# Optimization experiments

Measured on AMD Instinct MI355X. Metric: run time of the kernel, lower is better.

Reference implementation:

```python
import jax, jax.numpy as jnp
from jax import lax
import numpy as np
import math

N = 8
IN_CH = 3
EPS = 1e-6


def _dct_basis(n=N):
    # basis[u, i] = c(u) * cos(pi * u * (i + 0.5) / n)
    u = np.arange(n)
    i = np.arange(n)
    b = np.cos(np.pi * np.outer(u, i + 0.5) / n)
    c = np.full(n, math.sqrt(2.0 / n))
    c[0] = math.sqrt(1.0 / n)
    return b * c[:, None]


def _dct_conv_weight(n=N, in_ch=IN_CH):
    # weight[k = u*n + v, i, j] = basis[u,i] * basis[v,j]; grouped conv OIHW with I=1
    b = _dct_basis(n)
    w = np.einsum('ui,vj->uvij', b, b).reshape(n * n, 1, n, n).astype(np.float32)
    return np.concatenate([w] * in_ch, axis=0)  # [in_ch*n*n, 1, n, n]


def setup_inputs() -> dict:
    key = jax.random.key(0)
    k1, k2, k3 = jax.random.split(key, 3)
    B, C, H, W = 32, 3, 512, 512
    x = jax.random.uniform(k1, (B, C, H, W), dtype=jnp.float32)  # RGB in [0,1)
    # per-(sample, channel) stats; keep divisor d = max - min + eps > 1 so the
    # B-times repeated in-place normalization of the original stays finite
    max_ = 1.5 + jax.random.uniform(k2, (B, C * N * N, 1, 1), dtype=jnp.float32)
    min_ = 0.1 * jax.random.uniform(k3, (B, C * N * N, 1, 1), dtype=jnp.float32)
    ycbcr_w = jnp.asarray(
        [[0.299, 0.587, 0.114],
         [-0.169, -0.331, 0.5],
         [0.5, -0.419, -0.081]], dtype=jnp.float32)  # [out_c, in_c]
    dct_w = jnp.asarray(_dct_conv_weight())  # [192, 1, 8, 8]
    return {"x": x, "max_": max_, "min_": min_, "ycbcr_w": ycbcr_w, "dct_w": dct_w}


def reference(x, max_, min_, ycbcr_w, dct_w):
    # 1x1 RGB -> YCbCr conv == channel matmul
    ycbcr = jnp.einsum('oc,bchw->bohw', ycbcr_w, x)
    # grouped 8x8 stride-8 block-DCT conv: [B, 192, H/8, W/8]
    dct = lax.conv_general_dilated(
        ycbcr, dct_w, window_strides=(N, N), padding='VALID',
        feature_group_count=IN_CH,
        dimension_numbers=('NCHW', 'OIHW', 'NCHW'))
    # Original applies t = (t - min) / (max - min + eps) in-place B times per
    # sample (outer loop index i is unused but repeats the whole inner loop).
    d = max_ - min_ + EPS
    B = x.shape[0]
    out = lax.fori_loop(0, B, lambda i, t: (t - min_) / d, dct)
    return out
```

## Files before the change

### kernel.cpp

```cpp
#include <hip/hip_runtime.h>


#define HW 512
#define CHST (HW * HW)
#define NPAIR 6144
#define EPS 1e-6f

static constexpr float BASIS[8][8] = {
  { 0.35355339059327373f, 0.35355339059327373f, 0.35355339059327373f, 0.35355339059327373f,
    0.35355339059327373f, 0.35355339059327373f, 0.35355339059327373f, 0.35355339059327373f },
  { 0.49039264020161522f, 0.41573480615127262f, 0.27778511650980114f, 0.09754516100806412f,
   -0.09754516100806412f,-0.27778511650980114f,-0.41573480615127262f,-0.49039264020161522f },
  { 0.46193976625564337f, 0.19134171618254492f,-0.19134171618254492f,-0.46193976625564337f,
   -0.46193976625564337f,-0.19134171618254492f, 0.19134171618254492f, 0.46193976625564337f },
  { 0.41573480615127262f,-0.09754516100806412f,-0.49039264020161522f,-0.27778511650980114f,
    0.27778511650980114f, 0.49039264020161522f, 0.09754516100806412f,-0.41573480615127262f },
  { 0.35355339059327373f,-0.35355339059327373f,-0.35355339059327373f, 0.35355339059327373f,
    0.35355339059327373f,-0.35355339059327373f,-0.35355339059327373f, 0.35355339059327373f },
  { 0.27778511650980114f,-0.49039264020161522f, 0.09754516100806412f, 0.41573480615127262f,
   -0.41573480615127262f,-0.09754516100806412f, 0.49039264020161522f,-0.27778511650980114f },
  { 0.19134171618254492f,-0.46193976625564337f, 0.46193976625564337f,-0.19134171618254492f,
   -0.19134171618254492f, 0.46193976625564337f,-0.46193976625564337f, 0.19134171618254492f },
  { 0.09754516100806412f,-0.27778511650980114f, 0.41573480615127262f,-0.49039264020161522f,
    0.49039264020161522f,-0.41573480615127262f, 0.27778511650980114f,-0.09754516100806412f }
};

__global__ void precomp_norm(const float* __restrict__ max_,
                             const float* __restrict__ min_,
                             float* __restrict__ so) {
    int i = blockIdx.x * 256 + threadIdx.x;
    if (i >= NPAIR) return;
    float mn = min_[i], mx = max_[i];
    float d = mx - mn + EPS;
    float a = 1.0f / d;
    float a2 = a * a, a4 = a2 * a2, a8 = a4 * a4, a16 = a8 * a8, a32 = a16 * a16;
    float geo = a * (1.0f - a32) / (1.0f - a);
    so[2 * i]     = a32;
    so[2 * i + 1] = -mn * geo;
}

template <bool USE_WS>
__global__ __launch_bounds__(256)
void dct_kernel(const float* __restrict__ x,
                const float* __restrict__ ycbcr_w,
                const float* __restrict__ so,
                const float* __restrict__ max_,
                const float* __restrict__ min_,
                float* __restrict__ out) {
    __shared__ float ylds[3 * 8 * HW];

    const int b  = blockIdx.x >> 6;
    const int by = blockIdx.x & 63;
    const int t  = threadIdx.x;

    const float* band = x + (size_t)(b * 3) * CHST + (by * 8) * HW;

    float w00 = ycbcr_w[0], w01 = ycbcr_w[1], w02 = ycbcr_w[2];
    float w10 = ycbcr_w[3], w11 = ycbcr_w[4], w12 = ycbcr_w[5];
    float w20 = ycbcr_w[6], w21 = ycbcr_w[7], w22 = ycbcr_w[8];

    float4 Rv[4], Gv[4], Bv[4];
#pragma unroll
    for (int w = 0; w < 4; ++w) {
        const int o = t + 256 * w;
        Rv[w] = ((const float4*)(band))[o];
        Gv[w] = ((const float4*)(band + CHST))[o];
        Bv[w] = ((const float4*)(band + 2 * CHST))[o];
    }
    float4* yv = (float4*)ylds;
#pragma unroll
    for (int w = 0; w < 4; ++w) {
        const int o = t + 256 * w;
        float4 y0, y1, y2;
        y0.x = fmaf(w00, Rv[w].x, fmaf(w01, Gv[w].x, w02 * Bv[w].x));
        y0.y = fmaf(w00, Rv[w].y, fmaf(w01, Gv[w].y, w02 * Bv[w].y));
        y0.z = fmaf(w00, Rv[w].z, fmaf(w01, Gv[w].z, w02 * Bv[w].z));
        y0.w = fmaf(w00, Rv[w].w, fmaf(w01, Gv[w].w, w02 * Bv[w].w));
        y1.x = fmaf(w10, Rv[w].x, fmaf(w11, Gv[w].x, w12 * Bv[w].x));
        y1.y = fmaf(w10, Rv[w].y, fmaf(w11, Gv[w].y, w12 * Bv[w].y));
        y1.z = fmaf(w10, Rv[w].z, fmaf(w11, Gv[w].z, w12 * Bv[w].z));
        y1.w = fmaf(w10, Rv[w].w, fmaf(w11, Gv[w].w, w12 * Bv[w].w));
        y2.x = fmaf(w20, Rv[w].x, fmaf(w21, Gv[w].x, w22 * Bv[w].x));
        y2.y = fmaf(w20, Rv[w].y, fmaf(w21, Gv[w].y, w22 * Bv[w].y));
        y2.z = fmaf(w20, Rv[w].z, fmaf(w21, Gv[w].z, w22 * Bv[w].z));
        y2.w = fmaf(w20, Rv[w].w, fmaf(w21, Gv[w].w, w22 * Bv[w].w));
        yv[o]          = y0;
        yv[1024 + o]   = y1;
        yv[2048 + o]   = y2;
    }
    __syncthreads();

    if (t < 192) {
        const int c  = t >> 6;
        const int bx = t & 63;

        const float* yl = ylds + c * (8 * HW) + bx * 8;

        float tmp[8][8];
#pragma unroll
        for (int u = 0; u < 8; ++u)
#pragma unroll
            for (int j = 0; j < 8; ++j) tmp[u][j] = 0.0f;

#pragma unroll
        for (int i = 0; i < 8; ++i) {
            float y[8];
            *(float4*)(&y[0]) = *(const float4*)(yl + i * HW);
            *(float4*)(&y[4]) = *(const float4*)(yl + i * HW + 4);
#pragma unroll
            for (int u = 0; u < 8; ++u) {
                const float bu = BASIS[u][i];
#pragma unroll
                for (int j = 0; j < 8; ++j)
                    tmp[u][j] = fmaf(bu, y[j], tmp[u][j]);
            }
        }

        const int obase = b * 192 + c * 64;
        float* op = out + ((size_t)obase * 64 + by) * 64 + bx;

#pragma unroll
        for (int u = 0; u < 8; ++u) {
#pragma unroll
            for (int v = 0; v < 8; ++v) {
                float acc = tmp[u][0] * BASIS[v][0];
#pragma unroll
                for (int j = 1; j < 8; ++j)
                    acc = fmaf(tmp[u][j], BASIS[v][j], acc);
                const int k = u * 8 + v;
                float s, o;
                if (USE_WS) {
                    s = so[(obase + k) * 2];
                    o = so[(obase + k) * 2 + 1];
                } else {
                    float mn = min_[obase + k], mx = max_[obase + k];
                    float d  = mx - mn + EPS;
                    float a  = 1.0f / d;
                    float a2 = a * a, a4 = a2 * a2, a8 = a4 * a4, a16 = a8 * a8, a32 = a16 * a16;
                    s = a32;
                    o = -mn * (a * (1.0f - a32) / (1.0f - a));
                }
                op[(size_t)k * 4096] = fmaf(s, acc, o);
            }
        }
    }
}

extern "C" void kernel_launch(void* const* d_in, const int* in_sizes, int n_in,
                              void* d_out, int out_size, void* d_ws, size_t ws_size,
                              hipStream_t stream) {
    const float* x    = (const float*)d_in[0];
    const float* max_ = (const float*)d_in[1];
    const float* min_ = (const float*)d_in[2];
    const float* yw   = (const float*)d_in[3];
    float* out = (float*)d_out;
    float* so  = (float*)d_ws;

    const bool use_ws = (ws_size >= (size_t)NPAIR * 2 * sizeof(float));
    if (use_ws) {
        precomp_norm<<<(NPAIR + 255) / 256, 256, 0, stream>>>(max_, min_, so);
        dct_kernel<true><<<32 * 64, 256, 0, stream>>>(x, yw, so, max_, min_, out);
    } else {
        dct_kernel<false><<<32 * 64, 256, 0, stream>>>(x, yw, nullptr, max_, min_, out);
    }
}
```

Baseline: 185.6 us.

## Drop LDS staging; each thread loads RGB directly and computes its own YCbCr channel

Removes the 48KB shared-memory Y band and the block barrier. Each of 192 threads now reads its 8x8 RGB block straight from global memory and applies its own channel's YCbCr weights before the row DCT. This lowers LDS use and allows more resident blocks per CU, but every RGB pixel is now loaded three times (once per output channel, mostly hitting cache) and the per-thread loads are strided rather than fully coalesced. It also packs the scale/offset pair into a single float2 load.

```diff
diff --git a/kernel.cpp b/kernel.cpp
--- a/kernel.cpp
+++ b/kernel.cpp
@@ -40,108 +40,87 @@
 }
 
 template <bool USE_WS>
-__global__ __launch_bounds__(256)
+__global__ __launch_bounds__(192, 4)
 void dct_kernel(const float* __restrict__ x,
                 const float* __restrict__ ycbcr_w,
                 const float* __restrict__ so,
                 const float* __restrict__ max_,
                 const float* __restrict__ min_,
                 float* __restrict__ out) {
-    __shared__ float ylds[3 * 8 * HW];
-
     const int b  = blockIdx.x >> 6;
     const int by = blockIdx.x & 63;
     const int t  = threadIdx.x;
+    const int c  = t >> 6;
+    const int bx = t & 63;
 
-    const float* band = x + (size_t)(b * 3) * CHST + (by * 8) * HW;
+    const float wr = ycbcr_w[3 * c];
+    const float wg = ycbcr_w[3 * c + 1];
+    const float wb = ycbcr_w[3 * c + 2];
 
-    float w00 = ycbcr_w[0], w01 = ycbcr_w[1], w02 = ycbcr_w[2];
-    float w10 = ycbcr_w[3], w11 = ycbcr_w[4], w12 = ycbcr_w[5];
-    float w20 = ycbcr_w[6], w21 = ycbcr_w[7], w22 = ycbcr_w[8];
+    const float* base = x + (size_t)(b * 3) * CHST + (size_t)(by * 8) * HW + bx * 8;
 
-    float4 Rv[4], Gv[4], Bv[4];
+    float tmp[8][8];
 #pragma unroll
-    for (int w = 0; w < 4; ++w) {
-        const int o = t + 256 * w;
-        Rv[w] = ((const float4*)(band))[o];
-        Gv[w] = ((const float4*)(band + CHST))[o];
-        Bv[w] = ((const float4*)(band + 2 * CHST))[o];
-    }
-    float4* yv = (float4*)ylds;
+    for (int u = 0; u < 8; ++u)
 #pragma unroll
-    for (int w = 0; w < 4; ++w) {
-        const int o = t + 256 * w;
-        float4 y0, y1, y2;
-        y0.x = fmaf(w00, Rv[w].x, fmaf(w01, Gv[w].x, w02 * Bv[w].x));
-        y0.y = fmaf(w00, Rv[w].y, fmaf(w01, Gv[w].y, w02 * Bv[w].y));
-        y0.z = fmaf(w00, Rv[w].z, fmaf(w01, Gv[w].z, w02 * Bv[w].z));
-        y0.w = fmaf(w00, Rv[w].w, fmaf(w01, Gv[w].w, w02 * Bv[w].w));
-        y1.x = fmaf(w10, Rv[w].x, fmaf(w11, Gv[w].x, w12 * Bv[w].x));
-        y1.y = fmaf(w10, Rv[w].y, fmaf(w11, Gv[w].y, w12 * Bv[w].y));
-        y1.z = fmaf(w10, Rv[w].z, fmaf(w11, Gv[w].z, w12 * Bv[w].z));
-        y1.w = fmaf(w10, Rv[w].w, fmaf(w11, Gv[w].w, w12 * Bv[w].w));
-        y2.x = fmaf(w20, Rv[w].x, fmaf(w21, Gv[w].x, w22 * Bv[w].x));
-        y2.y = fmaf(w20, Rv[w].y, fmaf(w21, Gv[w].y, w22 * Bv[w].y));
-        y2.z = fmaf(w20, Rv[w].z, fmaf(w21, Gv[w].z, w22 * Bv[w].z));
-        y2.w = fmaf(w20, Rv[w].w, fmaf(w21, Gv[w].w, w22 * Bv[w].w));
-        yv[o]          = y0;
-        yv[1024 + o]   = y1;
-        yv[2048 + o]   = y2;
-    }
-    __syncthreads();
-
-    if (t < 192) {
-        const int c  = t >> 6;
-        const int bx = t & 63;
-
-        const float* yl = ylds + c * (8 * HW) + bx * 8;
-
-        float tmp[8][8];
-#pragma unroll
-        for (int u = 0; u < 8; ++u)
-#pragma unroll
-            for (int j = 0; j < 8; ++j) tmp[u][j] = 0.0f;
+        for (int j = 0; j < 8; ++j) tmp[u][j] = 0.0f;
 
 #pragma unroll
-        for (int i = 0; i < 8; ++i) {
-            float y[8];
-            *(float4*)(&y[0]) = *(const float4*)(yl + i * HW);
-            *(float4*)(&y[4]) = *(const float4*)(yl + i * HW + 4);
-#pragma unroll
-            for (int u = 0; u < 8; ++u) {
-                const float bu = BASIS[u][i];
-#pragma unroll
-                for (int j = 0; j < 8; ++j)
-                    tmp[u][j] = fmaf(bu, y[j], tmp[u][j]);
-            }
-        }
+    for (int i = 0; i < 8; ++i) {
+        const float* rp = base + i * HW;
+        float4 r0 = *(const float4*)(rp);
+        float4 r1 = *(const float4*)(rp + 4);
+        float4 g0 = *(const float4*)(rp + CHST);
+        float4 g1 = *(const float4*)(rp + CHST + 4);
+        float4 b0 = *(const float4*)(rp + 2 * CHST);
+        float4 b1 = *(const float4*)(rp + 2 * CHST + 4);
 
-        const int obase = b * 192 + c * 64;
-        float* op = out + ((size_t)obase * 64 + by) * 64 + bx;
+        float y[8];
+        y[0] = fmaf(wr, r0.x, fmaf(wg, g0.x, wb * b0.x));
+        y[1] = fmaf(wr, r0.y, fmaf(wg, g0.y, wb * b0.y));
+        y[2] = fmaf(wr, r0.z, fmaf(wg, g0.z, wb * b0.z));
+        y[3] = fmaf(wr, r0.w, fmaf(wg, g0.w, wb * b0.w));
+        y[4] = fmaf(wr, r1.x, fmaf(wg, g1.x, wb * b1.x));
+        y[5] = fmaf(wr, r1.y, fmaf(wg, g1.y, wb * b1.y));
+        y[6] = fmaf(wr, r1.z, fmaf(wg, g1.z, wb * b1.z));
+        y[7] = fmaf(wr, r1.w, fmaf(wg, g1.w, wb * b1.w));
 
 #pragma unroll
         for (int u = 0; u < 8; ++u) {
+            const float bu = BASIS[u][i];
 #pragma unroll
-            for (int v = 0; v < 8; ++v) {
-                float acc = tmp[u][0] * BASIS[v][0];
+            for (int j = 0; j < 8; ++j)
+                tmp[u][j] = fmaf(bu, y[j], tmp[u][j]);
+        }
+    }
+
+    const int obase = b * 192 + c * 64;
+    float* op = out + ((size_t)obase * 64 + by) * 64 + bx;
+    const float2* sop = (const float2*)so + obase;
+
 #pragma unroll
-                for (int j = 1; j < 8; ++j)
-                    acc = fmaf(tmp[u][j], BASIS[v][j], acc);
-                const int k = u * 8 + v;
-                float s, o;
-                if (USE_WS) {
-                    s = so[(obase + k) * 2];
-                    o = so[(obase + k) * 2 + 1];
-                } else {
-                    float mn = min_[obase + k], mx = max_[obase + k];
-                    float d  = mx - mn + EPS;
-                    float a  = 1.0f / d;
-                    float a2 = a * a, a4 = a2 * a2, a8 = a4 * a4, a16 = a8 * a8, a32 = a16 * a16;
-                    s = a32;
-                    o = -mn * (a * (1.0f - a32) / (1.0f - a));
-                }
-                op[(size_t)k * 4096] = fmaf(s, acc, o);
+    for (int u = 0; u < 8; ++u) {
+#pragma unroll
+        for (int v = 0; v < 8; ++v) {
+            float acc = tmp[u][0] * BASIS[v][0];
+#pragma unroll
+            for (int j = 1; j < 8; ++j)
+                acc = fmaf(tmp[u][j], BASIS[v][j], acc);
+            const int k = u * 8 + v;
+            float s, o;
+            if (USE_WS) {
+                float2 p = sop[k];
+                s = p.x;
+                o = p.y;
+            } else {
+                float mn = min_[obase + k], mx = max_[obase + k];
+                float d  = mx - mn + EPS;
+                float a  = 1.0f / d;
+                float a2 = a * a, a4 = a2 * a2, a8 = a4 * a4, a16 = a8 * a8, a32 = a16 * a16;
+                s = a32;
+                o = -mn * (a * (1.0f - a32) / (1.0f - a));
             }
+            op[(size_t)k * 4096] = fmaf(s, acc, o);
         }
     }
 }
@@ -159,8 +138,8 @@
     const bool use_ws = (ws_size >= (size_t)NPAIR * 2 * sizeof(float));
     if (use_ws) {
         precomp_norm<<<(NPAIR + 255) / 256, 256, 0, stream>>>(max_, min_, so);
-        dct_kernel<true><<<32 * 64, 256, 0, stream>>>(x, yw, so, max_, min_, out);
+        dct_kernel<true><<<32 * 64, 192, 0, stream>>>(x, yw, so, max_, min_, out);
     } else {
-        dct_kernel<false><<<32 * 64, 256, 0, stream>>>(x, yw, nullptr, max_, min_, out);
+        dct_kernel<false><<<32 * 64, 192, 0, stream>>>(x, yw, nullptr, max_, min_, out);
     }
 }
```

Measured after the change: 202.1 us. 1.09x slower.
